# Performance work log

Hardware: AMD Instinct MI355X
Metric: run time of the kernel (lower is better)

Reference implementation:

```python
import jax, jax.numpy as jnp
import numpy as np

EPS = 1e-5
NUM_LAYERS = 3


def _batchnorm(h, g, b):
    mean = h.mean(axis=0)
    var = h.var(axis=0)  # biased variance, matches torch BatchNorm training math
    return (h - mean) * jax.lax.rsqrt(var + EPS) * g + b


def setup_inputs() -> dict:
    key = jax.random.key(0)
    ks = jax.random.split(key, 8)
    N, E, D, H, OUT = 100000, 1600000, 128, 128, 64
    s = 0.08  # weight scale for numerical sanity
    return {
        "x": jax.random.normal(ks[0], (N, D), jnp.float32),
        "edge_index": jax.random.randint(ks[1], (2, E), 0, N, jnp.int64),
        "Wl": jax.random.normal(ks[2], (NUM_LAYERS, D, H), jnp.float32) * s,
        "bl": jnp.zeros((NUM_LAYERS, H), jnp.float32),
        "Wr": jax.random.normal(ks[3], (NUM_LAYERS, D, H), jnp.float32) * s,
        "gamma": jnp.ones((NUM_LAYERS, H), jnp.float32),
        "beta": jnp.zeros((NUM_LAYERS, H), jnp.float32),
        "W1": jax.random.normal(ks[4], (D + NUM_LAYERS * H, 2 * OUT), jnp.float32) * s,
        "b1": jnp.zeros((2 * OUT,), jnp.float32),
        "g1": jnp.ones((2 * OUT,), jnp.float32),
        "be1": jnp.zeros((2 * OUT,), jnp.float32),
        "W2": jax.random.normal(ks[5], (2 * OUT, OUT), jnp.float32) * s,
        "b2": jnp.zeros((OUT,), jnp.float32),
    }


def reference(x, edge_index, Wl, bl, Wr, gamma, beta, W1, b1, g1, be1, W2, b2):
    # GraphSAGE: stacked SAGEConv(mean aggr) + BatchNorm + ReLU, JK-concat, 2-layer MLP head.
    # Dropout is identity (eval mode).
    N = x.shape[0]
    src, dst = edge_index[0], edge_index[1]
    deg = jax.ops.segment_sum(jnp.ones((src.shape[0],), x.dtype), dst, num_segments=N)
    inv_deg = (1.0 / jnp.maximum(deg, 1.0))[:, None]  # [N,1]
    xs = [x]
    h = x
    for i in range(NUM_LAYERS):
        # mean-aggregate neighbor features, then linear (same math as PyG SAGEConv)
        agg = jax.ops.segment_sum(h[src], dst, num_segments=N) * inv_deg  # [N,D]
        h = agg @ Wl[i] + bl[i] + h @ Wr[i]
        h = _batchnorm(h, gamma[i], beta[i])
        h = jax.nn.relu(h)
        xs.append(h)
    z = jnp.concatenate(xs, axis=-1)  # [N, D + L*H]
    z = _batchnorm(z @ W1 + b1, g1, be1)
    z = jax.nn.leaky_relu(z, negative_slope=0.01)
    return z @ W2 + b2
```

## Files before the change

### kernel.cpp

```cpp
#include <hip/hip_runtime.h>
#include <hip/hip_bf16.h>

#define CDIV(a,b) (((a)+(b)-1)/(b))

typedef __attribute__((ext_vector_type(8))) short short8_t;
typedef __attribute__((ext_vector_type(4))) float f32x4;

__device__ __forceinline__ float b2f(ushort u){
    union { uint i; float f; } v; v.i = ((uint)u) << 16; return v.f;
}
__device__ __forceinline__ ushort f2b(float f){
    __hip_bfloat16 h = __float2bfloat16(f);
    return *reinterpret_cast<ushort*>(&h);
}

__global__ __launch_bounds__(256) void k_bcount(
    const int* __restrict__ dst, int E, int nbuck, int* __restrict__ bcnt)
{
    __shared__ int cnt[512];
    const int t = threadIdx.x;
    for (int i = t; i < nbuck; i += 256) cnt[i] = 0;
    __syncthreads();
    const int e0 = blockIdx.x * 4096;
    #pragma unroll
    for (int q = 0; q < 16; ++q){
        int idx = e0 + q*256 + t;
        if (idx < E) atomicAdd(&cnt[dst[idx] >> 8], 1);
    }
    __syncthreads();
    for (int i = t; i < nbuck; i += 256){
        int c = cnt[i];
        if (c) atomicAdd(&bcnt[i], c);
    }
}

__global__ void k_bscan(const int* __restrict__ bcnt, int nbuck, int E,
                        int* __restrict__ bbase, int* __restrict__ gcur)
{
    __shared__ int s[512];
    int t = threadIdx.x;
    int v = (t < nbuck) ? bcnt[t] : 0;
    s[t] = v;
    __syncthreads();
    for (int off = 1; off < 512; off <<= 1){
        int x = (t >= off) ? s[t-off] : 0;
        __syncthreads();
        s[t] += x;
        __syncthreads();
    }
    if (t < nbuck){ int e = s[t] - v; bbase[t] = e; gcur[t] = e; }
    if (t == 0) bbase[nbuck] = E;
}

__global__ __launch_bounds__(256) void k_bucketA(
    const int* __restrict__ src, const int* __restrict__ dst, int E,
    int nbuck, int* __restrict__ gcur, uint* __restrict__ ebuf)
{
    __shared__ int cnt[512];
    __shared__ int base[512];
    const int t  = threadIdx.x;
    const int e0 = blockIdx.x * 4096;
    for (int i = t; i < nbuck; i += 256) cnt[i] = 0;
    __syncthreads();
    uint pk[16]; int mb[16];
    #pragma unroll
    for (int q = 0; q < 16; ++q){
        int idx = e0 + q*256 + t;
        int b = -1; uint pkv = 0;
        if (idx < E){
            int s = src[idx], d = dst[idx];
            b = d >> 8;
            pkv = (uint)s | ((uint)(d & 255) << 24);
            atomicAdd(&cnt[b], 1);
        }
        mb[q] = b; pk[q] = pkv;
    }
    __syncthreads();
    for (int i = t; i < nbuck; i += 256){
        int c = cnt[i];
        base[i] = c ? atomicAdd(&gcur[i], c) : 0;
    }
    __syncthreads();
    for (int i = t; i < nbuck; i += 256) cnt[i] = 0;
    __syncthreads();
    #pragma unroll
    for (int q = 0; q < 16; ++q){
        if (mb[q] >= 0){
            int b   = mb[q];
            int pos = base[b] + atomicAdd(&cnt[b], 1);
            ebuf[pos] = pk[q];
        }
    }
}

__global__ __launch_bounds__(256) void k_build(
    const uint* __restrict__ ebuf, const int* __restrict__ bbase,
    int N, int E, int* __restrict__ row_ptr, float* __restrict__ inv_deg,
    int* __restrict__ col_idx)
{
    __shared__ int cnt[256];
    __shared__ int scn[256];
    const int b = blockIdx.x;
    const int t = threadIdx.x;
    const int n0 = b << 8;
    const int ebase = bbase[b], eend = bbase[b+1];

    cnt[t] = 0;
    __syncthreads();
    for (int j = ebase + t; j < eend; j += 256)
        atomicAdd(&cnt[ebuf[j] >> 24], 1);
    __syncthreads();

    int d = cnt[t];
    scn[t] = d;
    __syncthreads();
    for (int off = 1; off < 256; off <<= 1){
        int x = (t >= off) ? scn[t-off] : 0;
        __syncthreads();
        scn[t] += x;
        __syncthreads();
    }
    int excl = scn[t] - d;
    int node = n0 + t;
    if (node < N){
        row_ptr[node] = ebase + excl;
        inv_deg[node] = 1.0f / (float)(d > 1 ? d : 1);
    }
    if (b == 0 && t == 0) row_ptr[N] = E;

    cnt[t] = excl;
    __syncthreads();
    for (int j = ebase + t; j < eend; j += 256){
        uint e = ebuf[j];
        int p = atomicAdd(&cnt[e >> 24], 1);
        col_idx[ebase + p] = (int)(e & 0xFFFFFFu);
    }
}

__global__ void k_cvt_x(const float* __restrict__ in, ushort* __restrict__ out, int n4){
    int i = blockIdx.x*blockDim.x + threadIdx.x;
    if (i >= n4) return;
    float4 v = reinterpret_cast<const float4*>(in)[i];
    ushort4 o; o.x=f2b(v.x); o.y=f2b(v.y); o.z=f2b(v.z); o.w=f2b(v.w);
    reinterpret_cast<ushort4*>(out)[i] = o;
}

__global__ void k_cvt_t(const float* __restrict__ in, ushort* __restrict__ out,
                        int K, int C, int total){
    int i = blockIdx.x*blockDim.x + threadIdx.x;
    if (i >= total) return;
    int kc = K*C;
    int s = i / kc, r = i - s*kc;
    int k = r / C, c = r - k*C;
    out[s*kc + c*K + k] = f2b(in[i]);
}

template<int NORM>
__global__ __launch_bounds__(256) void k_agg_bf(
    const ushort* __restrict__ h, const int* __restrict__ row_ptr,
    const int* __restrict__ col_idx, const float* __restrict__ inv_deg,
    const float* __restrict__ ssp, ushort* __restrict__ agg, int N)
{
    int node = (blockIdx.x*blockDim.x + threadIdx.x) >> 6;
    int lane = threadIdx.x & 63;
    if (node >= N) return;
    const int g = lane >> 4, l15 = lane & 15;
    const int beg = row_ptr[node], end = row_ptr[node+1];
    const size_t co = (size_t)l15 * 8;

    float scv[8], shv[8];
    if (NORM){
        float4 c0 = *reinterpret_cast<const float4*>(ssp + co);
        float4 c1 = *reinterpret_cast<const float4*>(ssp + co + 4);
        float4 s0 = *reinterpret_cast<const float4*>(ssp + 128 + co);
        float4 s1 = *reinterpret_cast<const float4*>(ssp + 128 + co + 4);
        scv[0]=c0.x; scv[1]=c0.y; scv[2]=c0.z; scv[3]=c0.w;
        scv[4]=c1.x; scv[5]=c1.y; scv[6]=c1.z; scv[7]=c1.w;
        shv[0]=s0.x; shv[1]=s0.y; shv[2]=s0.z; shv[3]=s0.w;
        shv[4]=s1.x; shv[5]=s1.y; shv[6]=s1.z; shv[7]=s1.w;
    }

    float2 a2[4];
    #pragma unroll
    for (int q = 0; q < 4; ++q) a2[q] = make_float2(0.f, 0.f);

    auto acc8 = [&](uint4 v){
        uint w[4] = {v.x, v.y, v.z, v.w};
        #pragma unroll
        for (int q = 0; q < 4; ++q){
            union { uint i; float f; } lo, hi;
            lo.i = w[q] << 16;
            hi.i = w[q] & 0xffff0000u;
            float fl = lo.f, fh = hi.f;
            if (NORM){
                fl = fmaxf(fl*scv[2*q]   + shv[2*q],   0.f);
                fh = fmaxf(fh*scv[2*q+1] + shv[2*q+1], 0.f);
            }
            a2[q].x += fl;
            a2[q].y += fh;
        }
    };

    int j = beg + g;
    for (; j + 12 < end; j += 16){
        int i0 = col_idx[j], i1 = col_idx[j+4], i2 = col_idx[j+8], i3 = col_idx[j+12];
        uint4 v0 = *reinterpret_cast<const uint4*>(h + (size_t)i0*128 + co);
        uint4 v1 = *reinterpret_cast<const uint4*>(h + (size_t)i1*128 + co);
        uint4 v2 = *reinterpret_cast<const uint4*>(h + (size_t)i2*128 + co);
        uint4 v3 = *reinterpret_cast<const uint4*>(h + (size_t)i3*128 + co);
        acc8(v0); acc8(v1); acc8(v2); acc8(v3);
    }
    for (; j < end; j += 4){
        int i0 = col_idx[j];
        uint4 v0 = *reinterpret_cast<const uint4*>(h + (size_t)i0*128 + co);
        acc8(v0);
    }

    #pragma unroll
    for (int q = 0; q < 4; ++q){
        a2[q].x += __shfl_xor(a2[q].x, 16);
        a2[q].y += __shfl_xor(a2[q].y, 16);
        a2[q].x += __shfl_xor(a2[q].x, 32);
        a2[q].y += __shfl_xor(a2[q].y, 32);
    }

    if (g == 0){
        float sc = inv_deg[node];
        uint r[4];
        #pragma unroll
        for (int q = 0; q < 4; ++q)
            r[q] = (uint)f2b(a2[q].x*sc) | ((uint)f2b(a2[q].y*sc) << 16);
        *reinterpret_cast<uint4*>(agg + (size_t)node*128 + co) =
            make_uint4(r[0], r[1], r[2], r[3]);
    }
}

__device__ __forceinline__ short8_t norm_frag(short8_t a, const float* __restrict__ sp,
                                              int kbase, int leaky)
{
    float4 c0 = *reinterpret_cast<const float4*>(sp + kbase);
    float4 c1 = *reinterpret_cast<const float4*>(sp + kbase + 4);
    float4 h0 = *reinterpret_cast<const float4*>(sp + 128 + kbase);
    float4 h1 = *reinterpret_cast<const float4*>(sp + 128 + kbase + 4);
    float cs[8] = {c0.x,c0.y,c0.z,c0.w,c1.x,c1.y,c1.z,c1.w};
    float hs[8] = {h0.x,h0.y,h0.z,h0.w,h1.x,h1.y,h1.z,h1.w};
    uint* au = reinterpret_cast<uint*>(&a);
    short8_t r;
    uint* ru = reinterpret_cast<uint*>(&r);
    #pragma unroll
    for (int q = 0; q < 4; ++q){
        float lo = b2f((ushort)(au[q] & 0xffffu));
        float hi = b2f((ushort)(au[q] >> 16));
        lo = lo*cs[2*q]   + hs[2*q];
        hi = hi*cs[2*q+1] + hs[2*q+1];
        if (leaky){ lo = lo > 0.f ? lo : 0.01f*lo; hi = hi > 0.f ? hi : 0.01f*hi; }
        else      { lo = fmaxf(lo, 0.f); hi = fmaxf(hi, 0.f); }
        ru[q] = (uint)f2b(lo) | ((uint)f2b(hi) << 16);
    }
    return r;
}

template<int NCF, int STATS, int OUTBF>
__global__ __launch_bounds__(256) void k_gemm_mfma(
    const ushort* __restrict__ A0, const ushort* __restrict__ T0,
    const ushort* __restrict__ A1, const ushort* __restrict__ T1,
    const ushort* __restrict__ A2, const ushort* __restrict__ T2,
    const ushort* __restrict__ A3, const ushort* __restrict__ T3,
    const float* __restrict__ ns0, const float* __restrict__ ns1,
    const float* __restrict__ ns2, const float* __restrict__ ns3,
    int m0, int m1, int m2, int m3,
    int P, const float* __restrict__ bias,
    ushort* __restrict__ out_bf, float* __restrict__ out_f32,
    float* __restrict__ partials, int N)
{
    __shared__ ushort Ws[NCF*16*128];
    const int t   = threadIdx.x;
    const int w   = t >> 6, l = t & 63;
    const int l15 = l & 15, lg = l >> 4;
    const int r0   = blockIdx.x * 128;
    const int wrow = w * 32;

    f32x4 acc[2][NCF];
    #pragma unroll
    for (int i = 0; i < 2; ++i)
        #pragma unroll
        for (int j = 0; j < NCF; ++j) acc[i][j] = (f32x4){0.f,0.f,0.f,0.f};

    for (int p = 0; p < P; ++p){
        const ushort* A  = (p==0)?A0:(p==1)?A1:(p==2)?A2:A3;
        const ushort* T  = (p==0)?T0:(p==1)?T1:(p==2)?T2:T3;
        const float*  ns = (p==0)?ns0:(p==1)?ns1:(p==2)?ns2:ns3;
        const int     md = (p==0)?m0:(p==1)?m1:(p==2)?m2:m3;
        if (p) __syncthreads();
        #pragma unroll
        for (int q = 0; q < NCF; ++q){
            int lin  = q*256 + t;
            int row  = lin >> 4, c16 = lin & 15;
            int c16s = c16 ^ (row & 7);
            uint4 v = *reinterpret_cast<const uint4*>(T + (size_t)row*128 + c16*8);
            *reinterpret_cast<uint4*>(&Ws[row*128 + c16s*8]) = v;
        }
        __syncthreads();
        #pragma unroll
        for (int kk = 0; kk < 4; ++kk){
            const int k0 = kk*32;
            short8_t a[2];
            #pragma unroll
            for (int rf = 0; rf < 2; ++rf){
                size_t gr = (size_t)(r0 + wrow + rf*16 + l15);
                a[rf] = *reinterpret_cast<const short8_t*>(A + gr*128 + k0 + lg*8);
            }
            if (md){
                a[0] = norm_frag(a[0], ns, k0 + lg*8, md == 2);
                a[1] = norm_frag(a[1], ns, k0 + lg*8, md == 2);
            }
            #pragma unroll
            for (int cf = 0; cf < NCF; ++cf){
                int row  = cf*16 + l15;
                int c16  = (k0 >> 3) + lg;
                int c16s = c16 ^ (row & 7);
                short8_t b = *reinterpret_cast<const short8_t*>(&Ws[row*128 + c16s*8]);
                acc[0][cf] = __builtin_amdgcn_mfma_f32_16x16x32_bf16(a[0], b, acc[0][cf], 0, 0, 0);
                acc[1][cf] = __builtin_amdgcn_mfma_f32_16x16x32_bf16(a[1], b, acc[1][cf], 0, 0, 0);
            }
        }
    }

    float bs[NCF];
    #pragma unroll
    for (int cf = 0; cf < NCF; ++cf) bs[cf] = bias[cf*16 + l15];

    float s1[NCF], s2[NCF];
    #pragma unroll
    for (int cf = 0; cf < NCF; ++cf){ s1[cf] = 0.f; s2[cf] = 0.f; }

    #pragma unroll
    for (int rf = 0; rf < 2; ++rf){
        #pragma unroll
        for (int q = 0; q < 4; ++q){
            int gr = r0 + wrow + rf*16 + lg*4 + q;
            bool valid = gr < N;
            #pragma unroll
            for (int cf = 0; cf < NCF; ++cf){
                float v = acc[rf][cf][q] + bs[cf];
                if (valid){
                    if (STATS){ s1[cf] += v; s2[cf] += v*v; }
                    int col = cf*16 + l15;
                    if (OUTBF) out_bf[(size_t)gr*(NCF*16) + col] = f2b(v);
                    else       out_f32[(size_t)gr*(NCF*16) + col] = v;
                }
            }
        }
    }
    if (STATS){
        #pragma unroll
        for (int cf = 0; cf < NCF; ++cf){
            s1[cf] += __shfl_xor(s1[cf], 16);
            s1[cf] += __shfl_xor(s1[cf], 32);
            s2[cf] += __shfl_xor(s2[cf], 16);
            s2[cf] += __shfl_xor(s2[cf], 32);
        }
        if (l < 16){
            float* pb = partials + (size_t)(blockIdx.x*4 + w)*256;
            #pragma unroll
            for (int cf = 0; cf < NCF; ++cf){
                pb[cf*16 + l15]       = s1[cf];
                pb[128 + cf*16 + l15] = s2[cf];
            }
        }
    }
}

__global__ void k_bnreduce(const float* __restrict__ partials, int I, int N,
                           const float* __restrict__ gamma, const float* __restrict__ beta,
                           float* __restrict__ ss)
{
    int c = blockIdx.x;
    int l = threadIdx.x;
    float s1 = 0.f, s2 = 0.f;
    for (int i = l; i < I; i += 64){
        s1 += partials[(size_t)i*256 + c];
        s2 += partials[(size_t)i*256 + 128 + c];
    }
    #pragma unroll
    for (int off = 32; off; off >>= 1){
        s1 += __shfl_xor(s1, off);
        s2 += __shfl_xor(s2, off);
    }
    if (l == 0){
        float m   = s1 / (float)N;
        float var = s2 / (float)N - m*m;
        float sc  = rsqrtf(var + 1e-5f) * gamma[c];
        ss[c]     = sc;
        ss[128+c] = beta[c] - m*sc;
    }
}

extern "C" void kernel_launch(void* const* d_in, const int* in_sizes, int n_in,
                              void* d_out, int out_size, void* d_ws, size_t ws_size,
                              hipStream_t stream)
{
    const float* x     = (const float*)d_in[0];
    const int*   ei    = (const int*)  d_in[1];
    const float* Wl    = (const float*)d_in[2];
    const float* bl    = (const float*)d_in[3];
    const float* Wr    = (const float*)d_in[4];
    const float* gamma = (const float*)d_in[5];
    const float* beta  = (const float*)d_in[6];
    const float* W1    = (const float*)d_in[7];
    const float* b1    = (const float*)d_in[8];
    const float* g1    = (const float*)d_in[9];
    const float* be1   = (const float*)d_in[10];
    const float* W2    = (const float*)d_in[11];
    const float* b2    = (const float*)d_in[12];
    float* out = (float*)d_out;

    const int N  = in_sizes[0] / 128;
    const int E  = in_sizes[1] / 2;
    const int NB = CDIV(N, 128);
    const size_t NPAD = (size_t)NB * 128;
    const int* src = ei;
    const int* dst = ei + E;

    const int NBUCK = CDIV(N, 256);

    char* w = (char*)d_ws;
    const size_t SB = NPAD * 128 * sizeof(ushort);
    ushort* x_bf = (ushort*)(w + 0*SB);
    ushort* pre0 = (ushort*)(w + 1*SB);
    ushort* pre1 = (ushort*)(w + 2*SB);
    ushort* pre2 = (ushort*)(w + 3*SB);
    ushort* aggb = (ushort*)(w + 4*SB);
    ushort* preh = (ushort*)(w + 5*SB);
    char* p = w + 6*SB;
    ushort* WtL = (ushort*)p;  p += (size_t)3*16384*2;
    ushort* WtR = (ushort*)p;  p += (size_t)3*16384*2;
    ushort* Wt1 = (ushort*)p;  p += (size_t)4*16384*2;
    ushort* Wt2 = (ushort*)p;  p += (size_t)8192*2;
    float* partials = (float*)p; p += (size_t)NB*4*256*sizeof(float);
    uint*  ebuf     = (uint*)p;  p += (size_t)E*4;
    int*   col_idx  = (int*)p;   p += (size_t)E*4;
    int*   row_ptr  = (int*)p;   p += (size_t)(N+1)*4;
    float* inv_deg  = (float*)p; p += (size_t)N*4;
    int*   bcnt     = (int*)p;   p += 512*4;
    int*   bbase    = (int*)p;   p += 516*4;
    int*   gcur     = (int*)p;   p += 512*4;
    float* ss0      = (float*)p; p += 256*4;
    float* ss1      = (float*)p; p += 256*4;
    float* ss2      = (float*)p; p += 256*4;
    float* ssh      = (float*)p; p += 256*4;

    const int n4 = N * 32;
    k_cvt_x<<<CDIV(n4,256), 256, 0, stream>>>(x, x_bf, n4);
    k_cvt_t<<<CDIV(3*16384,256), 256, 0, stream>>>(Wl, WtL, 128, 128, 3*16384);
    k_cvt_t<<<CDIV(3*16384,256), 256, 0, stream>>>(Wr, WtR, 128, 128, 3*16384);
    k_cvt_t<<<CDIV(4*16384,256), 256, 0, stream>>>(W1, Wt1, 128, 128, 4*16384);
    k_cvt_t<<<CDIV(8192,256),    256, 0, stream>>>(W2, Wt2, 128,  64, 8192);

    hipMemsetAsync(bcnt, 0, 512*4, stream);
    k_bcount<<<CDIV(E,4096), 256, 0, stream>>>(dst, E, NBUCK, bcnt);
    k_bscan<<<1, 512, 0, stream>>>(bcnt, NBUCK, E, bbase, gcur);
    k_bucketA<<<CDIV(E,4096), 256, 0, stream>>>(src, dst, E, NBUCK, gcur, ebuf);
    k_build<<<NBUCK, 256, 0, stream>>>(ebuf, bbase, N, E, row_ptr, inv_deg, col_idx);

    ushort* pre[3] = {pre0, pre1, pre2};
    float*  ssl[3] = {ss0, ss1, ss2};
    const int I = NB * 4;

    for (int L = 0; L < 3; ++L){
        if (L == 0)
            k_agg_bf<0><<<CDIV(N,4), 256, 0, stream>>>(x_bf, row_ptr, col_idx, inv_deg,
                                                       nullptr, aggb, N);
        else
            k_agg_bf<1><<<CDIV(N,4), 256, 0, stream>>>(pre[L-1], row_ptr, col_idx, inv_deg,
                                                       ssl[L-1], aggb, N);
        const ushort* hsrc = (L == 0) ? x_bf : pre[L-1];
        const float*  hns  = (L == 0) ? nullptr : ssl[L-1];
        int hmode = (L == 0) ? 0 : 1;
        k_gemm_mfma<8,1,1><<<NB, 256, 0, stream>>>(
            aggb, WtL + (size_t)L*16384,
            hsrc, WtR + (size_t)L*16384,
            nullptr, nullptr, nullptr, nullptr,
            nullptr, hns, nullptr, nullptr,
            0, hmode, 0, 0,
            2, bl + (size_t)L*128, pre[L], nullptr, partials, N);
        k_bnreduce<<<128, 64, 0, stream>>>(partials, I, N,
            gamma + (size_t)L*128, beta + (size_t)L*128, ssl[L]);
    }

    k_gemm_mfma<8,1,1><<<NB, 256, 0, stream>>>(
        x_bf, Wt1 + 0,
        pre0, Wt1 + 16384,
        pre1, Wt1 + 2*16384,
        pre2, Wt1 + 3*16384,
        nullptr, ss0, ss1, ss2,
        0, 1, 1, 1,
        4, b1, preh, nullptr, partials, N);
    k_bnreduce<<<128, 64, 0, stream>>>(partials, I, N, g1, be1, ssh);

    k_gemm_mfma<4,0,0><<<NB, 256, 0, stream>>>(
        preh, Wt2, nullptr, nullptr, nullptr, nullptr, nullptr, nullptr,
        ssh, nullptr, nullptr, nullptr,
        2, 0, 0, 0,
        1, b2, nullptr, out, partials, N);
}
```

Measured before the change: 517.4 us.

## Load GEMM weight fragments into registers instead of LDS, reduce aggregation unroll

The GEMM kernel drops the shared-memory weight tile and its barriers. Each lane now loads its B fragments for all K steps directly from global memory into registers, and all A fragments are loaded up front with a paired normalisation helper. It also sets launch bounds to 2 blocks per CU. The aggregation gather loop is reduced from 4-way to 2-way unrolling. This removes LDS staging and syncs, but raises register pressure (NCF*4 + 8 short8 fragments) and means redundant global or L2 weight reads across waves, while the aggregation has less memory-level parallelism.

New measurement: 641.3 us. 24.0% more time.

```diff
diff --git a/kernel.cpp b/kernel.cpp
--- a/kernel.cpp
+++ b/kernel.cpp
@@ -202,17 +202,17 @@
     };
 
     int j = beg + g;
-    for (; j + 12 < end; j += 16){
-        int i0 = col_idx[j], i1 = col_idx[j+4], i2 = col_idx[j+8], i3 = col_idx[j+12];
-        uint4 v0 = *reinterpret_cast<const uint4*>(h + (size_t)i0*128 + co);
-        uint4 v1 = *reinterpret_cast<const uint4*>(h + (size_t)i1*128 + co);
-        uint4 v2 = *reinterpret_cast<const uint4*>(h + (size_t)i2*128 + co);
-        uint4 v3 = *reinterpret_cast<const uint4*>(h + (size_t)i3*128 + co);
-        acc8(v0); acc8(v1); acc8(v2); acc8(v3);
-    }
-    for (; j < end; j += 4){
-        int i0 = col_idx[j];
-        uint4 v0 = *reinterpret_cast<const uint4*>(h + (size_t)i0*128 + co);
+    while (j + 4 < end){
+        int s0 = col_idx[j];
+        int s1 = col_idx[j+4];
+        uint4 v0 = *reinterpret_cast<const uint4*>(h + (size_t)s0*128 + co);
+        uint4 v1 = *reinterpret_cast<const uint4*>(h + (size_t)s1*128 + co);
+        acc8(v0); acc8(v1);
+        j += 8;
+    }
+    if (j < end){
+        int s0 = col_idx[j];
+        uint4 v0 = *reinterpret_cast<const uint4*>(h + (size_t)s0*128 + co);
         acc8(v0);
     }
 
@@ -235,8 +235,9 @@
     }
 }
 
-__device__ __forceinline__ short8_t norm_frag(short8_t a, const float* __restrict__ sp,
-                                              int kbase, int leaky)
+__device__ __forceinline__ void norm_frag2(short8_t& a0, short8_t& a1,
+                                           const float* __restrict__ sp,
+                                           int kbase, int leaky)
 {
     float4 c0 = *reinterpret_cast<const float4*>(sp + kbase);
     float4 c1 = *reinterpret_cast<const float4*>(sp + kbase + 4);
@@ -244,24 +245,28 @@
     float4 h1 = *reinterpret_cast<const float4*>(sp + 128 + kbase + 4);
     float cs[8] = {c0.x,c0.y,c0.z,c0.w,c1.x,c1.y,c1.z,c1.w};
     float hs[8] = {h0.x,h0.y,h0.z,h0.w,h1.x,h1.y,h1.z,h1.w};
-    uint* au = reinterpret_cast<uint*>(&a);
-    short8_t r;
-    uint* ru = reinterpret_cast<uint*>(&r);
+    uint* u0 = reinterpret_cast<uint*>(&a0);
+    uint* u1 = reinterpret_cast<uint*>(&a1);
     #pragma unroll
     for (int q = 0; q < 4; ++q){
-        float lo = b2f((ushort)(au[q] & 0xffffu));
-        float hi = b2f((ushort)(au[q] >> 16));
-        lo = lo*cs[2*q]   + hs[2*q];
-        hi = hi*cs[2*q+1] + hs[2*q+1];
-        if (leaky){ lo = lo > 0.f ? lo : 0.01f*lo; hi = hi > 0.f ? hi : 0.01f*hi; }
-        else      { lo = fmaxf(lo, 0.f); hi = fmaxf(hi, 0.f); }
-        ru[q] = (uint)f2b(lo) | ((uint)f2b(hi) << 16);
-    }
-    return r;
+        float lo0 = b2f((ushort)(u0[q] & 0xffffu)) * cs[2*q]   + hs[2*q];
+        float hi0 = b2f((ushort)(u0[q] >> 16))     * cs[2*q+1] + hs[2*q+1];
+        float lo1 = b2f((ushort)(u1[q] & 0xffffu)) * cs[2*q]   + hs[2*q];
+        float hi1 = b2f((ushort)(u1[q] >> 16))     * cs[2*q+1] + hs[2*q+1];
+        if (leaky){
+            lo0 = lo0 > 0.f ? lo0 : 0.01f*lo0;  hi0 = hi0 > 0.f ? hi0 : 0.01f*hi0;
+            lo1 = lo1 > 0.f ? lo1 : 0.01f*lo1;  hi1 = hi1 > 0.f ? hi1 : 0.01f*hi1;
+        } else {
+            lo0 = fmaxf(lo0, 0.f); hi0 = fmaxf(hi0, 0.f);
+            lo1 = fmaxf(lo1, 0.f); hi1 = fmaxf(hi1, 0.f);
+        }
+        u0[q] = (uint)f2b(lo0) | ((uint)f2b(hi0) << 16);
+        u1[q] = (uint)f2b(lo1) | ((uint)f2b(hi1) << 16);
+    }
 }
 
 template<int NCF, int STATS, int OUTBF>
-__global__ __launch_bounds__(256) void k_gemm_mfma(
+__global__ __launch_bounds__(256, 2) void k_gemm_regb(
     const ushort* __restrict__ A0, const ushort* __restrict__ T0,
     const ushort* __restrict__ A1, const ushort* __restrict__ T1,
     const ushort* __restrict__ A2, const ushort* __restrict__ T2,
@@ -273,7 +278,6 @@
     ushort* __restrict__ out_bf, float* __restrict__ out_f32,
     float* __restrict__ partials, int N)
 {
-    __shared__ ushort Ws[NCF*16*128];
     const int t   = threadIdx.x;
     const int w   = t >> 6, l = t & 63;
     const int l15 = l & 15, lg = l >> 4;
@@ -291,39 +295,36 @@
         const ushort* T  = (p==0)?T0:(p==1)?T1:(p==2)?T2:T3;
         const float*  ns = (p==0)?ns0:(p==1)?ns1:(p==2)?ns2:ns3;
         const int     md = (p==0)?m0:(p==1)?m1:(p==2)?m2:m3;
-        if (p) __syncthreads();
-        #pragma unroll
-        for (int q = 0; q < NCF; ++q){
-            int lin  = q*256 + t;
-            int row  = lin >> 4, c16 = lin & 15;
-            int c16s = c16 ^ (row & 7);
-            uint4 v = *reinterpret_cast<const uint4*>(T + (size_t)row*128 + c16*8);
-            *reinterpret_cast<uint4*>(&Ws[row*128 + c16s*8]) = v;
-        }
-        __syncthreads();
-        #pragma unroll
-        for (int kk = 0; kk < 4; ++kk){
-            const int k0 = kk*32;
-            short8_t a[2];
+
+        short8_t B[NCF][4];
+        #pragma unroll
+        for (int cf = 0; cf < NCF; ++cf)
+            #pragma unroll
+            for (int kk = 0; kk < 4; ++kk)
+                B[cf][kk] = *reinterpret_cast<const short8_t*>(
+                    T + (size_t)(cf*16 + l15)*128 + kk*32 + lg*8);
+
+        short8_t af[4][2];
+        #pragma unroll
+        for (int kk = 0; kk < 4; ++kk)
             #pragma unroll
             for (int rf = 0; rf < 2; ++rf){
                 size_t gr = (size_t)(r0 + wrow + rf*16 + l15);
-                a[rf] = *reinterpret_cast<const short8_t*>(A + gr*128 + k0 + lg*8);
+                af[kk][rf] = *reinterpret_cast<const short8_t*>(
+                    A + gr*128 + kk*32 + lg*8);
             }
-            if (md){
-                a[0] = norm_frag(a[0], ns, k0 + lg*8, md == 2);
-                a[1] = norm_frag(a[1], ns, k0 + lg*8, md == 2);
-            }
+        if (md){
+            #pragma unroll
+            for (int kk = 0; kk < 4; ++kk)
+                norm_frag2(af[kk][0], af[kk][1], ns, kk*32 + lg*8, md == 2);
+        }
+        #pragma unroll
+        for (int kk = 0; kk < 4; ++kk)
             #pragma unroll
             for (int cf = 0; cf < NCF; ++cf){
-                int row  = cf*16 + l15;
-                int c16  = (k0 >> 3) + lg;
-                int c16s = c16 ^ (row & 7);
-                short8_t b = *reinterpret_cast<const short8_t*>(&Ws[row*128 + c16s*8]);
-                acc[0][cf] = __builtin_amdgcn_mfma_f32_16x16x32_bf16(a[0], b, acc[0][cf], 0, 0, 0);
-                acc[1][cf] = __builtin_amdgcn_mfma_f32_16x16x32_bf16(a[1], b, acc[1][cf], 0, 0, 0);
+                acc[0][cf] = __builtin_amdgcn_mfma_f32_16x16x32_bf16(af[kk][0], B[cf][kk], acc[0][cf], 0, 0, 0);
+                acc[1][cf] = __builtin_amdgcn_mfma_f32_16x16x32_bf16(af[kk][1], B[cf][kk], acc[1][cf], 0, 0, 0);
             }
-        }
     }
 
     float bs[NCF];
@@ -477,7 +478,7 @@
         const ushort* hsrc = (L == 0) ? x_bf : pre[L-1];
         const float*  hns  = (L == 0) ? nullptr : ssl[L-1];
         int hmode = (L == 0) ? 0 : 1;
-        k_gemm_mfma<8,1,1><<<NB, 256, 0, stream>>>(
+        k_gemm_regb<8,1,1><<<NB, 256, 0, stream>>>(
             aggb, WtL + (size_t)L*16384,
             hsrc, WtR + (size_t)L*16384,
             nullptr, nullptr, nullptr, nullptr,
@@ -488,7 +489,7 @@
             gamma + (size_t)L*128, beta + (size_t)L*128, ssl[L]);
     }
 
-    k_gemm_mfma<8,1,1><<<NB, 256, 0, stream>>>(
+    k_gemm_regb<8,1,1><<<NB, 256, 0, stream>>>(
         x_bf, Wt1 + 0,
         pre0, Wt1 + 16384,
         pre1, Wt1 + 2*16384,
@@ -498,7 +499,7 @@
         4, b1, preh, nullptr, partials, N);
     k_bnreduce<<<128, 64, 0, stream>>>(partials, I, N, g1, be1, ssh);
 
-    k_gemm_mfma<4,0,0><<<NB, 256, 0, stream>>>(
+    k_gemm_regb<4,0,0><<<NB, 256, 0, stream>>>(
         preh, Wt2, nullptr, nullptr, nullptr, nullptr, nullptr, nullptr,
         ssh, nullptr, nullptr, nullptr,
         2, 0, 0, 0,
```
